# Optimization experiments

Hardware: AMD Instinct MI355X
Metric: run time of the kernel (lower is better)

## Reference

```python
import jax, jax.numpy as jnp
import numpy as np

SCALE = 8.0  # (dim // n_heads) ** 0.5 = (1024 // 16) ** 0.5


def setup_inputs() -> dict:
    key = jax.random.key(0)
    kq, kk, kv = jax.random.split(key, 3)
    shape = (2, 16, 2048, 64)  # [B, H, N, Dh]
    q = jax.random.normal(kq, shape, dtype=jnp.float32)
    k = jax.random.normal(kk, shape, dtype=jnp.float32)
    v = jax.random.normal(kv, shape, dtype=jnp.float32)
    return {"q": q, "k": k, "v": v}


def reference(q, k, v):
    # scores[b,h,n,m] = sum_d q[b,h,n,d] * k[b,h,m,d], then MULTIPLIED by scale
    # (the original multiplies by sqrt(head_dim), it does not divide).
    scores = jnp.einsum('bhnd,bhmd->bhnm', q, k) * SCALE
    scores = jax.nn.softmax(scores, axis=-1)
    # Faithful to the original quirky einsum: sums over n (query axis), keeps m.
    # out[b,h,m,d] = (sum_n scores[b,h,n,m]) * v[b,h,m,d]
    out = jnp.einsum('bhnm,bhmd->bhmd', scores, v)
    return out
```

## Files before the change

kernel.cpp:

```cpp
#include <hip/hip_runtime.h>
#include <math.h>

#define BH 32
#define NN 2048
#define DD 64
#define BHNN (BH * NN)
#define QK ((size_t)BH * NN * DD)
#define LDK 72

#define QSCALE 11.5415603f

typedef __attribute__((ext_vector_type(8)))  _Float16 halfx8;
typedef __attribute__((ext_vector_type(4)))  _Float16 halfx4;
typedef __attribute__((ext_vector_type(16))) float    floatx16;

__device__ inline float fexp2(float x) { return __builtin_amdgcn_exp2f(x); }

__device__ inline int rowmap(int r, int half) {
    return (r & 3) + 8 * (r >> 2) + 4 * half;
}

__global__ __launch_bounds__(256) void convert_kernel(const float4* __restrict__ q,
                                                      const float4* __restrict__ k,
                                                      _Float16* __restrict__ qhi,
                                                      _Float16* __restrict__ qlo,
                                                      _Float16* __restrict__ khi) {
    size_t gid = (size_t)blockIdx.x * 256 + threadIdx.x;
    float4 qa = q[gid];
    float4 ka = k[gid];
    float qf[4] = {qa.x, qa.y, qa.z, qa.w};
    float kf[4] = {ka.x, ka.y, ka.z, ka.w};
    halfx4 h, l, kh;
#pragma unroll
    for (int i = 0; i < 4; ++i) {
        float f = qf[i] * QSCALE;
        _Float16 hh = (_Float16)f;
        h[i] = hh;
        l[i] = (_Float16)(f - (float)hh);
        kh[i] = (_Float16)kf[i];
    }
    *(halfx4*)&qhi[gid * 4] = h;
    *(halfx4*)&qlo[gid * 4] = l;
    *(halfx4*)&khi[gid * 4] = kh;
}

__device__ inline void load_tile(const _Float16* __restrict__ khi_t,
                                 int tid, halfx8 rh[4]) {
#pragma unroll
    for (int i = 0; i < 4; ++i) {
        int c = tid + 256 * i;
        int r = c >> 3, s = c & 7;
        rh[i] = *(const halfx8*)&khi_t[(size_t)r * 64 + s * 8];
    }
}
__device__ inline void write_tile(_Float16* Khi, int tid, const halfx8 rh[4]) {
#pragma unroll
    for (int i = 0; i < 4; ++i) {
        int c = tid + 256 * i;
        int r = c >> 3, s = c & 7;
        *(halfx8*)&Khi[r * LDK + s * 8] = rh[i];
    }
}

__device__ inline void load_a(const _Float16* __restrict__ qhi_row,
                              const _Float16* __restrict__ qlo_row,
                              int half, halfx8 ah[4], halfx8 al[4]) {
#pragma unroll
    for (int ks = 0; ks < 4; ++ks) {
        ah[ks] = *(const halfx8*)&qhi_row[ks * 16 + half * 8];
        al[ks] = *(const halfx8*)&qlo_row[ks * 16 + half * 8];
    }
}

__global__ __launch_bounds__(256, 2) void stats_kernel(const _Float16* __restrict__ qhi,
                                                       const _Float16* __restrict__ qlo,
                                                       const _Float16* __restrict__ khi,
                                                       float* __restrict__ smax_p,
                                                       float* __restrict__ sden_p) {
    __shared__ _Float16 Khi[128 * LDK];
    const int g    = blockIdx.x & 63;
    const int bh   = g & 31;
    const int ms   = g >> 5;
    const int n0   = (blockIdx.x >> 6) * 128;
    const int tid  = threadIdx.x;
    const int wave = tid >> 6, lane = tid & 63;
    const int half = lane >> 5, l31 = lane & 31;
    const size_t base = (size_t)bh * NN * DD;

    halfx8 ah[4], al[4];
    {
        size_t ro = base + (size_t)(n0 + wave * 32 + l31) * DD;
        load_a(qhi + ro, qlo + ro, half, ah, al);
    }

    float m_run[16], d_run[16];
#pragma unroll
    for (int r = 0; r < 16; ++r) { m_run[r] = -INFINITY; d_run[r] = 0.f; }

    const _Float16* khi_b = khi + base;
    halfx8 rh[4];
    load_tile(khi_b + (size_t)(ms * 8) * 8192, tid, rh);

    for (int mti = 0; mti < 8; ++mti) {
        __syncthreads();
        write_tile(Khi, tid, rh);
        __syncthreads();
        if (mti < 7) {
            size_t toff = (size_t)(ms * 8 + mti + 1) * 8192;
            load_tile(khi_b + toff, tid, rh);
        }

        floatx16 acc[4];
#pragma unroll
        for (int t = 0; t < 4; ++t)
#pragma unroll
            for (int e = 0; e < 16; ++e) acc[t][e] = 0.f;

#pragma unroll
        for (int t = 0; t < 4; ++t) {
            const int mr = t * 32 + l31;
#pragma unroll
            for (int ks = 0; ks < 4; ++ks) {
                halfx8 bhf = *(const halfx8*)&Khi[mr * LDK + ks * 16 + half * 8];
                acc[t] = __builtin_amdgcn_mfma_f32_32x32x16_f16(ah[ks], bhf, acc[t], 0, 0, 0);
                acc[t] = __builtin_amdgcn_mfma_f32_32x32x16_f16(al[ks], bhf, acc[t], 0, 0, 0);
            }
        }

#pragma unroll
        for (int r = 0; r < 16; ++r) {
            float tmax = fmaxf(fmaxf(acc[0][r], acc[1][r]), fmaxf(acc[2][r], acc[3][r]));
            float m_new = fmaxf(m_run[r], tmax);
            float s = fexp2(acc[0][r] - m_new) + fexp2(acc[1][r] - m_new)
                    + fexp2(acc[2][r] - m_new) + fexp2(acc[3][r] - m_new);
            d_run[r] = d_run[r] * fexp2(m_run[r] - m_new) + s;
            m_run[r] = m_new;
        }
    }

    float* smp = smax_p + ((size_t)ms * BH + bh) * NN;
    float* sdp = sden_p + ((size_t)ms * BH + bh) * NN;
#pragma unroll
    for (int r = 0; r < 16; ++r) {
        float M = m_run[r];
#pragma unroll
        for (int off = 1; off < 32; off <<= 1)
            M = fmaxf(M, __shfl_xor(M, off));
        float dd = d_run[r] * fexp2(m_run[r] - M);
#pragma unroll
        for (int off = 1; off < 32; off <<= 1)
            dd += __shfl_xor(dd, off);
        if (l31 == 0) {
            int row = n0 + wave * 32 + rowmap(r, half);
            smp[row] = M;
            sdp[row] = dd;
        }
    }
}

__global__ __launch_bounds__(256) void combine_kernel(const float* __restrict__ smax_p,
                                                      const float* __restrict__ sden_p,
                                                      float* __restrict__ smaxC,
                                                      float* __restrict__ sinvC) {
    int idx = blockIdx.x * 256 + threadIdx.x;
    float m0 = smax_p[idx], m1 = smax_p[BHNN + idx];
    float d0 = sden_p[idx], d1 = sden_p[BHNN + idx];
    float M = fmaxf(m0, m1);
    float den = d0 * fexp2(m0 - M) + d1 * fexp2(m1 - M);
    smaxC[idx] = M;
    sinvC[idx] = 1.0f / den;
}

__global__ __launch_bounds__(256, 2) void wsum_kernel(const _Float16* __restrict__ qhi,
                                                      const _Float16* __restrict__ qlo,
                                                      const _Float16* __restrict__ khi,
                                                      const float* __restrict__ smaxC,
                                                      const float* __restrict__ sinvC,
                                                      float* __restrict__ wpart) {
    __shared__ _Float16 Khi[128 * LDK];
    __shared__ float wred[4 * 128];
    __shared__ float Ms[1024];
    __shared__ float Is[1024];
    const int g    = blockIdx.x & 63;
    const int bh   = g & 31;
    const int nz   = g >> 5;
    const int m0   = (blockIdx.x >> 6) * 128;
    const int tid  = threadIdx.x;
    const int wave = tid >> 6, lane = tid & 63;
    const int half = lane >> 5, l31 = lane & 31;
    const size_t base = (size_t)bh * NN * DD;

    {
        halfx8 rh[4];
        load_tile(khi + base + (size_t)m0 * 64, tid, rh);
        write_tile(Khi, tid, rh);
        const float4* sm4 = (const float4*)(smaxC + (size_t)bh * NN + nz * 1024);
        const float4* si4 = (const float4*)(sinvC + (size_t)bh * NN + nz * 1024);
        *(float4*)&Ms[tid * 4] = sm4[tid];
        *(float4*)&Is[tid * 4] = si4[tid];
    }
    __syncthreads();

    float wacc[4] = {0.f, 0.f, 0.f, 0.f};

#pragma unroll
    for (int it = 0; it < 8; ++it) {
        const int ls = wave + it * 4;
        halfx8 ah[4], al[4];
        {
            size_t ro = base + (size_t)((nz * 32 + ls) * 32 + l31) * DD;
            load_a(qhi + ro, qlo + ro, half, ah, al);
        }

        floatx16 acc[4];
#pragma unroll
        for (int t = 0; t < 4; ++t)
#pragma unroll
            for (int e = 0; e < 16; ++e) acc[t][e] = 0.f;

#pragma unroll
        for (int t = 0; t < 4; ++t) {
            const int mr = t * 32 + l31;
#pragma unroll
            for (int ks = 0; ks < 4; ++ks) {
                halfx8 bhf = *(const halfx8*)&Khi[mr * LDK + ks * 16 + half * 8];
                acc[t] = __builtin_amdgcn_mfma_f32_32x32x16_f16(ah[ks], bhf, acc[t], 0, 0, 0);
                acc[t] = __builtin_amdgcn_mfma_f32_32x32x16_f16(al[ks], bhf, acc[t], 0, 0, 0);
            }
        }

#pragma unroll
        for (int r = 0; r < 16; ++r) {
            const int lrow = ls * 32 + rowmap(r, half);
            float M   = Ms[lrow];
            float inv = Is[lrow];
#pragma unroll
            for (int t = 0; t < 4; ++t)
                wacc[t] += fexp2(acc[t][r] - M) * inv;
        }
    }

#pragma unroll
    for (int t = 0; t < 4; ++t) wacc[t] += __shfl_xor(wacc[t], 32);
    if (half == 0) {
#pragma unroll
        for (int t = 0; t < 4; ++t) wred[wave * 128 + t * 32 + l31] = wacc[t];
    }
    __syncthreads();
    if (tid < 128) {
        float s = wred[tid] + wred[128 + tid] + wred[256 + tid] + wred[384 + tid];
        wpart[((size_t)nz * BH + bh) * NN + m0 + tid] = s;
    }
}

__global__ __launch_bounds__(256) void out_kernel(const float* __restrict__ v,
                                                  const float* __restrict__ w0,
                                                  const float* __restrict__ w1,
                                                  float* __restrict__ out) {
    size_t gid = (size_t)blockIdx.x * 256 + threadIdx.x;
    const float4* v4 = (const float4*)v;
    float4* o4 = (float4*)out;
    float4 vv = v4[gid];
    float ww = w0[gid >> 4] + w1[gid >> 4];
    o4[gid] = make_float4(vv.x * ww, vv.y * ww, vv.z * ww, vv.w * ww);
}

extern "C" void kernel_launch(void* const* d_in, const int* in_sizes, int n_in,
                              void* d_out, int out_size, void* d_ws, size_t ws_size,
                              hipStream_t stream) {
    const float* q = (const float*)d_in[0];
    const float* k = (const float*)d_in[1];
    const float* v = (const float*)d_in[2];
    float* out = (float*)d_out;

    _Float16* qhi = (_Float16*)d_ws;
    _Float16* qlo = qhi + QK;
    _Float16* khi = qlo + QK;
    float* smax_p = (float*)(khi + QK);
    float* sden_p = smax_p + 2 * BHNN;
    float* smaxC  = sden_p + 2 * BHNN;
    float* sinvC  = smaxC + BHNN;
    float* wpart  = sinvC + BHNN;

    convert_kernel<<<QK / 4 / 256, 256, 0, stream>>>((const float4*)q, (const float4*)k,
                                                     qhi, qlo, khi);
    stats_kernel<<<1024, 256, 0, stream>>>(qhi, qlo, khi, smax_p, sden_p);
    combine_kernel<<<BHNN / 256, 256, 0, stream>>>(smax_p, sden_p, smaxC, sinvC);
    wsum_kernel<<<1024, 256, 0, stream>>>(qhi, qlo, khi, smaxC, sinvC, wpart);
    out_kernel<<<(BH * NN * DD / 4) / 256, 256, 0, stream>>>(v, wpart, wpart + BHNN, out);
}
```

Baseline: 190.9 us.

## Fold combine into wsum and halve accumulator tiles to raise occupancy

```diff
diff --git a/kernel.cpp b/kernel.cpp
--- a/kernel.cpp
+++ b/kernel.cpp
@@ -72,7 +72,7 @@
     }
 }
 
-__global__ __launch_bounds__(256, 2) void stats_kernel(const _Float16* __restrict__ qhi,
+__global__ __launch_bounds__(256, 4) void stats_kernel(const _Float16* __restrict__ qhi,
                                                        const _Float16* __restrict__ qlo,
                                                        const _Float16* __restrict__ khi,
                                                        float* __restrict__ smax_p,
@@ -110,31 +110,33 @@
             load_tile(khi_b + toff, tid, rh);
         }
 
-        floatx16 acc[4];
-#pragma unroll
-        for (int t = 0; t < 4; ++t)
-#pragma unroll
-            for (int e = 0; e < 16; ++e) acc[t][e] = 0.f;
-
-#pragma unroll
-        for (int t = 0; t < 4; ++t) {
-            const int mr = t * 32 + l31;
-#pragma unroll
-            for (int ks = 0; ks < 4; ++ks) {
-                halfx8 bhf = *(const halfx8*)&Khi[mr * LDK + ks * 16 + half * 8];
-                acc[t] = __builtin_amdgcn_mfma_f32_32x32x16_f16(ah[ks], bhf, acc[t], 0, 0, 0);
-                acc[t] = __builtin_amdgcn_mfma_f32_32x32x16_f16(al[ks], bhf, acc[t], 0, 0, 0);
-            }
-        }
-
-#pragma unroll
-        for (int r = 0; r < 16; ++r) {
-            float tmax = fmaxf(fmaxf(acc[0][r], acc[1][r]), fmaxf(acc[2][r], acc[3][r]));
-            float m_new = fmaxf(m_run[r], tmax);
-            float s = fexp2(acc[0][r] - m_new) + fexp2(acc[1][r] - m_new)
-                    + fexp2(acc[2][r] - m_new) + fexp2(acc[3][r] - m_new);
-            d_run[r] = d_run[r] * fexp2(m_run[r] - m_new) + s;
-            m_run[r] = m_new;
+#pragma unroll 1
+        for (int p = 0; p < 2; ++p) {
+            floatx16 acc[2];
+#pragma unroll
+            for (int t = 0; t < 2; ++t)
+#pragma unroll
+                for (int e = 0; e < 16; ++e) acc[t][e] = 0.f;
+
+#pragma unroll
+            for (int tt = 0; tt < 2; ++tt) {
+                const int mr = (p * 2 + tt) * 32 + l31;
+#pragma unroll
+                for (int ks = 0; ks < 4; ++ks) {
+                    halfx8 bhf = *(const halfx8*)&Khi[mr * LDK + ks * 16 + half * 8];
+                    acc[tt] = __builtin_amdgcn_mfma_f32_32x32x16_f16(ah[ks], bhf, acc[tt], 0, 0, 0);
+                    acc[tt] = __builtin_amdgcn_mfma_f32_32x32x16_f16(al[ks], bhf, acc[tt], 0, 0, 0);
+                }
+            }
+
+#pragma unroll
+            for (int r = 0; r < 16; ++r) {
+                float tmax = fmaxf(acc[0][r], acc[1][r]);
+                float m_new = fmaxf(m_run[r], tmax);
+                float s = fexp2(acc[0][r] - m_new) + fexp2(acc[1][r] - m_new);
+                d_run[r] = d_run[r] * fexp2(m_run[r] - m_new) + s;
+                m_run[r] = m_new;
+            }
         }
     }
 
@@ -158,24 +160,11 @@
     }
 }
 
-__global__ __launch_bounds__(256) void combine_kernel(const float* __restrict__ smax_p,
-                                                      const float* __restrict__ sden_p,
-                                                      float* __restrict__ smaxC,
-                                                      float* __restrict__ sinvC) {
-    int idx = blockIdx.x * 256 + threadIdx.x;
-    float m0 = smax_p[idx], m1 = smax_p[BHNN + idx];
-    float d0 = sden_p[idx], d1 = sden_p[BHNN + idx];
-    float M = fmaxf(m0, m1);
-    float den = d0 * fexp2(m0 - M) + d1 * fexp2(m1 - M);
-    smaxC[idx] = M;
-    sinvC[idx] = 1.0f / den;
-}
-
-__global__ __launch_bounds__(256, 2) void wsum_kernel(const _Float16* __restrict__ qhi,
+__global__ __launch_bounds__(256, 4) void wsum_kernel(const _Float16* __restrict__ qhi,
                                                       const _Float16* __restrict__ qlo,
                                                       const _Float16* __restrict__ khi,
-                                                      const float* __restrict__ smaxC,
-                                                      const float* __restrict__ sinvC,
+                                                      const float* __restrict__ smax_p,
+                                                      const float* __restrict__ sden_p,
                                                       float* __restrict__ wpart) {
     __shared__ _Float16 Khi[128 * LDK];
     __shared__ float wred[4 * 128];
@@ -194,16 +183,28 @@
         halfx8 rh[4];
         load_tile(khi + base + (size_t)m0 * 64, tid, rh);
         write_tile(Khi, tid, rh);
-        const float4* sm4 = (const float4*)(smaxC + (size_t)bh * NN + nz * 1024);
-        const float4* si4 = (const float4*)(sinvC + (size_t)bh * NN + nz * 1024);
-        *(float4*)&Ms[tid * 4] = sm4[tid];
-        *(float4*)&Is[tid * 4] = si4[tid];
+        size_t roff = (size_t)bh * NN + nz * 1024 + tid * 4;
+        float4 m0v = *(const float4*)&smax_p[roff];
+        float4 m1v = *(const float4*)&smax_p[(size_t)BHNN + roff];
+        float4 d0v = *(const float4*)&sden_p[roff];
+        float4 d1v = *(const float4*)&sden_p[(size_t)BHNN + roff];
+        float mm0[4] = {m0v.x, m0v.y, m0v.z, m0v.w};
+        float mm1[4] = {m1v.x, m1v.y, m1v.z, m1v.w};
+        float dd0[4] = {d0v.x, d0v.y, d0v.z, d0v.w};
+        float dd1[4] = {d1v.x, d1v.y, d1v.z, d1v.w};
+#pragma unroll
+        for (int j = 0; j < 4; ++j) {
+            float M = fmaxf(mm0[j], mm1[j]);
+            float den = dd0[j] * fexp2(mm0[j] - M) + dd1[j] * fexp2(mm1[j] - M);
+            Ms[tid * 4 + j] = M;
+            Is[tid * 4 + j] = 1.0f / den;
+        }
     }
     __syncthreads();
 
-    float wacc[4] = {0.f, 0.f, 0.f, 0.f};
-
-#pragma unroll
+    float wacc0 = 0.f, wacc1 = 0.f, wacc2 = 0.f, wacc3 = 0.f;
+
+#pragma unroll 1
     for (int it = 0; it < 8; ++it) {
         const int ls = wave + it * 4;
         halfx8 ah[4], al[4];
@@ -212,34 +213,40 @@
             load_a(qhi + ro, qlo + ro, half, ah, al);
         }
 
-        floatx16 acc[4];
-#pragma unroll
-        for (int t = 0; t < 4; ++t)
-#pragma unroll
-            for (int e = 0; e < 16; ++e) acc[t][e] = 0.f;
-
-#pragma unroll
-        for (int t = 0; t < 4; ++t) {
-            const int mr = t * 32 + l31;
-#pragma unroll
-            for (int ks = 0; ks < 4; ++ks) {
-                halfx8 bhf = *(const halfx8*)&Khi[mr * LDK + ks * 16 + half * 8];
-                acc[t] = __builtin_amdgcn_mfma_f32_32x32x16_f16(ah[ks], bhf, acc[t], 0, 0, 0);
-                acc[t] = __builtin_amdgcn_mfma_f32_32x32x16_f16(al[ks], bhf, acc[t], 0, 0, 0);
-            }
-        }
-
-#pragma unroll
-        for (int r = 0; r < 16; ++r) {
-            const int lrow = ls * 32 + rowmap(r, half);
-            float M   = Ms[lrow];
-            float inv = Is[lrow];
-#pragma unroll
-            for (int t = 0; t < 4; ++t)
-                wacc[t] += fexp2(acc[t][r] - M) * inv;
-        }
-    }
-
+#pragma unroll 1
+        for (int p = 0; p < 2; ++p) {
+            floatx16 acc[2];
+#pragma unroll
+            for (int t = 0; t < 2; ++t)
+#pragma unroll
+                for (int e = 0; e < 16; ++e) acc[t][e] = 0.f;
+
+#pragma unroll
+            for (int tt = 0; tt < 2; ++tt) {
+                const int mr = (p * 2 + tt) * 32 + l31;
+#pragma unroll
+                for (int ks = 0; ks < 4; ++ks) {
+                    halfx8 bhf = *(const halfx8*)&Khi[mr * LDK + ks * 16 + half * 8];
+                    acc[tt] = __builtin_amdgcn_mfma_f32_32x32x16_f16(ah[ks], bhf, acc[tt], 0, 0, 0);
+                    acc[tt] = __builtin_amdgcn_mfma_f32_32x32x16_f16(al[ks], bhf, acc[tt], 0, 0, 0);
+                }
+            }
+
+            float w0 = 0.f, w1 = 0.f;
+#pragma unroll
+            for (int r = 0; r < 16; ++r) {
+                const int lrow = ls * 32 + rowmap(r, half);
+                float M   = Ms[lrow];
+                float inv = Is[lrow];
+                w0 += fexp2(acc[0][r] - M) * inv;
+                w1 += fexp2(acc[1][r] - M) * inv;
+            }
+            if (p == 0) { wacc0 += w0; wacc1 += w1; }
+            else        { wacc2 += w0; wacc3 += w1; }
+        }
+    }
+
+    float wacc[4] = {wacc0, wacc1, wacc2, wacc3};
 #pragma unroll
     for (int t = 0; t < 4; ++t) wacc[t] += __shfl_xor(wacc[t], 32);
     if (half == 0) {
@@ -278,14 +285,11 @@
     _Float16* khi = qlo + QK;
     float* smax_p = (float*)(khi + QK);
     float* sden_p = smax_p + 2 * BHNN;
-    float* smaxC  = sden_p + 2 * BHNN;
-    float* sinvC  = smaxC + BHNN;
-    float* wpart  = sinvC + BHNN;
+    float* wpart  = sden_p + 2 * BHNN;
 
     convert_kernel<<<QK / 4 / 256, 256, 0, stream>>>((const float4*)q, (const float4*)k,
                                                      qhi, qlo, khi);
     stats_kernel<<<1024, 256, 0, stream>>>(qhi, qlo, khi, smax_p, sden_p);
-    combine_kernel<<<BHNN / 256, 256, 0, stream>>>(smax_p, sden_p, smaxC, sinvC);
-    wsum_kernel<<<1024, 256, 0, stream>>>(qhi, qlo, khi, smaxC, sinvC, wpart);
+    wsum_kernel<<<1024, 256, 0, stream>>>(qhi, qlo, khi, smax_p, sden_p, wpart);
     out_kernel<<<(BH * NN * DD / 4) / 256, 256, 0, stream>>>(v, wpart, wpart + BHNN, out);
 }
```

After: 205.5 us. 7.6% more time.
